# Kernel optimization log

Measured on AMD Instinct MI355X. Metric: run time of the kernel, lower is better.

## Reference

```python
import jax, jax.numpy as jnp
import numpy as np

N_NODES = 50000
BN_EPS = 1e-5


def gcn_conv(x, W, b, src, dst, ew):
    # x: [N, Fin], W: [Fin, Fout]; PyG GCNConv with self loops and edge weights
    xw = x @ W
    loop = jnp.arange(N_NODES)
    s = jnp.concatenate([src, loop])
    d = jnp.concatenate([dst, loop])
    w = jnp.concatenate([ew, jnp.ones((N_NODES,), ew.dtype)])
    deg = jax.ops.segment_sum(w, d, num_segments=N_NODES)
    dinv = jnp.where(deg > 0, jax.lax.rsqrt(deg), 0.0)
    norm = dinv[s] * w * dinv[d]                      # [E+N]
    msg = norm[:, None] * xw[s]                       # [E+N, Fout]
    out = jax.ops.segment_sum(msg, d, num_segments=N_NODES)
    return out + b


def batch_norm(x, gamma, beta):
    mu = jnp.mean(x, axis=0)
    var = jnp.mean(jnp.square(x - mu), axis=0)
    return gamma * (x - mu) * jax.lax.rsqrt(var + BN_EPS) + beta


def setup_inputs() -> dict:
    key = jax.random.key(0)
    ks = jax.random.split(key, 6)
    F_IN, H, C, E = 128, 128, 40, 800000
    x = jax.random.normal(ks[0], (N_NODES, F_IN), jnp.float32)
    edge_index = jax.random.randint(ks[1], (2, E), 0, N_NODES, jnp.int64)
    edge_weight = jax.random.uniform(ks[2], (E,), jnp.float32)
    W1 = jax.random.normal(ks[3], (F_IN, H), jnp.float32) / np.sqrt(F_IN)
    W2 = jax.random.normal(ks[4], (H, H), jnp.float32) / np.sqrt(H)
    W3 = jax.random.normal(ks[5], (H, C), jnp.float32) / np.sqrt(H)
    return {
        "x": x, "edge_index": edge_index, "edge_weight": edge_weight,
        "W1": W1, "b1": jnp.zeros((H,), jnp.float32),
        "gamma1": jnp.ones((H,), jnp.float32), "beta1": jnp.zeros((H,), jnp.float32),
        "W2": W2, "b2": jnp.zeros((H,), jnp.float32),
        "gamma2": jnp.ones((H,), jnp.float32), "beta2": jnp.zeros((H,), jnp.float32),
        "W3": W3, "b3": jnp.zeros((C,), jnp.float32),
    }


def reference(x, edge_index, edge_weight, W1, b1, gamma1, beta1,
              W2, b2, gamma2, beta2, W3, b3):
    src, dst = edge_index[0], edge_index[1]
    h = gcn_conv(x, W1, b1, src, dst, edge_weight)
    h = jax.nn.relu(batch_norm(h, gamma1, beta1))   # dropout = identity (eval)
    h = gcn_conv(h, W2, b2, src, dst, edge_weight)
    h = jax.nn.relu(batch_norm(h, gamma2, beta2))
    h = gcn_conv(h, W3, b3, src, dst, edge_weight)
    return jax.nn.log_softmax(h, axis=-1)
```

## Files before the change

kernel.cpp:

```cpp
#include <hip/hip_runtime.h>
#include <cstdint>
#include <cstddef>

#define N_NODES 50000
#define BN_EPS 1e-5f
#define NPB 256
#define NB ((N_NODES + NPB - 1) / NPB)
#define EPB 2048
#define BN_BLOCKS 128

typedef unsigned int uint32;
typedef unsigned short ushort;

typedef short bf16x8 __attribute__((ext_vector_type(8)));
typedef float f32x4 __attribute__((ext_vector_type(4)));


__device__ inline ushort bf16rn(float f) {
  unsigned int u = __float_as_uint(f);
  u += 0x7fffu + ((u >> 16) & 1u);
  return (ushort)(u >> 16);
}
__device__ inline float unbf(uint32 u) { return __uint_as_float(u << 16); }
__device__ inline float lo16(uint32 u) { return __uint_as_float(u << 16); }
__device__ inline float hi16(uint32 u) { return __uint_as_float(u & 0xffff0000u); }
__device__ inline uint32 pack2(float a, float b) {
  return (uint32)bf16rn(a) | ((uint32)bf16rn(b) << 16);
}


__global__ __launch_bounds__(256) void k_cvtW_all(const float* __restrict__ W1,
    const float* __restrict__ W2, const float* __restrict__ W3,
    ushort* __restrict__ Wt1, ushort* __restrict__ Wt2, ushort* __restrict__ Wt3) {
  int gid = blockIdx.x * 256 + threadIdx.x;
  if (gid < 16384) {
    int c = gid >> 7, k = gid & 127;
    Wt1[c * 128 + k] = bf16rn(W1[(size_t)k * 128 + c]);
  } else if (gid < 32768) {
    int g = gid - 16384, c = g >> 7, k = g & 127;
    Wt2[c * 128 + k] = bf16rn(W2[(size_t)k * 128 + c]);
  } else if (gid < 37888) {
    int g = gid - 32768, c = g >> 7, k = g & 127;
    Wt3[c * 128 + k] = bf16rn(W3[(size_t)k * 40 + c]);
  }
}


__global__ __launch_bounds__(256) void k_ehist(const int* __restrict__ dst, int E,
    int* __restrict__ histB, int* __restrict__ hists, int* __restrict__ done,
    int* __restrict__ rbase, int* __restrict__ cbase, int* __restrict__ start) {
  __shared__ int h[NB];
  for (int i = threadIdx.x; i < NB; i += 256) h[i] = 0;
  __syncthreads();
  int base = blockIdx.x * EPB;
  for (int i = threadIdx.x; i < EPB; i += 256) {
    int e = base + i;
    if (e < E) atomicAdd(&h[dst[e] >> 8], 1);
  }
  __syncthreads();
  for (int i = threadIdx.x; i < NB; i += 256) {
    int v = h[i];
    hists[blockIdx.x * NB + i] = v;
    if (v) atomicAdd(&histB[i], v);
  }
  if (threadIdx.x == 0) {
    __threadfence();
    int old = atomicAdd(done, 1);
    if (old == gridDim.x - 1) {
      __threadfence();
      int r = 0, c = 0;
      for (int b = 0; b < NB; ++b) {
        int npb = (b == NB - 1) ? (N_NODES - b * NPB) : NPB;
        rbase[b] = r; cbase[b] = c;
        r += histB[b]; c += histB[b] + npb;
      }
      rbase[NB] = r;
      start[N_NODES] = c;
    }
  }
}

__global__ __launch_bounds__(256) void k_binA(const int* __restrict__ src,
    const int* __restrict__ dst, const float* __restrict__ ew, int E,
    const int* __restrict__ rbase, const int* __restrict__ hists,
    int* __restrict__ gcur, uint2* __restrict__ bins) {
  __shared__ int gb[NB], cur[NB];
  for (int i = threadIdx.x; i < NB; i += 256) {
    int hv = hists[blockIdx.x * NB + i];
    cur[i] = 0;
    gb[i] = hv ? (rbase[i] + atomicAdd(&gcur[i], hv)) : 0;
  }
  __syncthreads();
  int base = blockIdx.x * EPB;
  for (int i = threadIdx.x; i < EPB; i += 256) {
    int e = base + i;
    if (e < E) {
      int d = dst[e];
      int g = d >> 8;
      int p = gb[g] + atomicAdd(&cur[g], 1);
      bins[p] = make_uint2((uint32)src[e] | ((uint32)(d & 255) << 16),
                           __float_as_uint(ew[e]));
    }
  }
}

__global__ __launch_bounds__(256) void k_binB(const uint2* __restrict__ bins,
    const int* __restrict__ rbase, const int* __restrict__ cbase,
    int* __restrict__ start, float* __restrict__ dinv, uint32* __restrict__ csr) {
  __shared__ int h[256], cur[256], ofs[256], sc[256];
  __shared__ float deg[256];
  int tid = threadIdx.x;
  int b = blockIdx.x;
  int node0 = b << 8;
  int npb = min(NPB, N_NODES - node0);
  h[tid] = 0; deg[tid] = 1.0f;
  __syncthreads();
  int r0 = rbase[b], r1 = rbase[b + 1];
  for (int i = r0 + tid; i < r1; i += 256) {
    uint2 rec = bins[i];
    int dl = (rec.x >> 16) & 255;
    atomicAdd(&h[dl], 1);
    atomicAdd(&deg[dl], __uint_as_float(rec.y));
  }
  __syncthreads();
  int v = (tid < npb) ? 1 + h[tid] : 0;
  sc[tid] = v;
  __syncthreads();
  for (int off = 1; off < 256; off <<= 1) {
    int a = (tid >= off) ? sc[tid - off] : 0;
    __syncthreads();
    sc[tid] += a;
    __syncthreads();
  }
  int cb = cbase[b];
  if (tid < npb) {
    int segBase = cb + sc[tid] - v;
    int node = node0 + tid;
    start[node] = segBase;
    csr[segBase] = (0x3F80u << 16) | (uint32)node;
    dinv[node] = rsqrtf(deg[tid]);
    ofs[tid] = segBase + 1;
    cur[tid] = 0;
  }
  __syncthreads();
  for (int i = r0 + tid; i < r1; i += 256) {
    uint2 rec = bins[i];
    int dl = (rec.x >> 16) & 255;
    int p = ofs[dl] + atomicAdd(&cur[dl], 1);
    csr[p] = ((uint32)bf16rn(__uint_as_float(rec.y)) << 16) | (rec.x & 0xffff);
  }
}

__global__ __launch_bounds__(256) void k_wnorm(uint32* __restrict__ csr,
    const int* __restrict__ start, const float* __restrict__ dinv) {
  int lane = threadIdx.x & 15;
  int node = blockIdx.x * 16 + (threadIdx.x >> 4);
  if (node >= N_NODES) return;
  float di = dinv[node];
  int e0 = start[node], e1 = start[node + 1];
  for (int e = e0 + lane; e < e1; e += 16) {
    uint32 c = csr[e];
    int s = c & 0xffff;
    float w = unbf(c >> 16) * dinv[s] * di;
    csr[e] = ((uint32)bf16rn(w) << 16) | (uint32)s;
  }
}


template <int BNT, typename XT>
__global__ __launch_bounds__(256) void k_mfma(const XT* __restrict__ X,
    const ushort* __restrict__ Wt, const float* __restrict__ ssb,
    ushort* __restrict__ out16, int Fout) {
  __shared__ ushort Xs[64][136];
  __shared__ ushort Bs[BNT * 16][136];
  int tid = threadIdx.x;
  int r0 = blockIdx.x * 64;

  for (int idx = tid; idx < BNT * 16 * 16; idx += 256) {
    int col = idx >> 4;
    int kk = (idx & 15) * 8;
    uint4 v = make_uint4(0, 0, 0, 0);
    if (col < Fout)
      v = *reinterpret_cast<const uint4*>(&Wt[(size_t)col * 128 + kk]);
    *reinterpret_cast<uint4*>(&Bs[col][kk]) = v;
  }

  if (sizeof(XT) == 4) {
    const float* Xf = reinterpret_cast<const float*>(X);
    for (int idx = tid; idx < 2048; idx += 256) {
      int row = idx >> 5;
      int kk = (idx & 31) * 4;
      int gr = r0 + row;
      float4 v = make_float4(0.f, 0.f, 0.f, 0.f);
      if (gr < N_NODES)
        v = *reinterpret_cast<const float4*>(&Xf[(size_t)gr * 128 + kk]);
      ushort4 o;
      o.x = bf16rn(v.x); o.y = bf16rn(v.y); o.z = bf16rn(v.z); o.w = bf16rn(v.w);
      *reinterpret_cast<ushort4*>(&Xs[row][kk]) = o;
    }
  } else {
    const ushort* X16 = reinterpret_cast<const ushort*>(X);
    for (int idx = tid; idx < 1024; idx += 256) {
      int row = idx >> 4;
      int kk = (idx & 15) * 8;
      int gr = r0 + row;
      uint4 v = make_uint4(0, 0, 0, 0);
      if (gr < N_NODES)
        v = *reinterpret_cast<const uint4*>(&X16[(size_t)gr * 128 + kk]);
      if (ssb) {
        float f[8] = { lo16(v.x), hi16(v.x), lo16(v.y), hi16(v.y),
                       lo16(v.z), hi16(v.z), lo16(v.w), hi16(v.w) };
        float4 sc0 = *reinterpret_cast<const float4*>(&ssb[kk]);
        float4 sc1 = *reinterpret_cast<const float4*>(&ssb[kk + 4]);
        float4 sh0 = *reinterpret_cast<const float4*>(&ssb[128 + kk]);
        float4 sh1 = *reinterpret_cast<const float4*>(&ssb[128 + kk + 4]);
        f[0] = fmaxf(0.f, f[0] * sc0.x + sh0.x);
        f[1] = fmaxf(0.f, f[1] * sc0.y + sh0.y);
        f[2] = fmaxf(0.f, f[2] * sc0.z + sh0.z);
        f[3] = fmaxf(0.f, f[3] * sc0.w + sh0.w);
        f[4] = fmaxf(0.f, f[4] * sc1.x + sh1.x);
        f[5] = fmaxf(0.f, f[5] * sc1.y + sh1.y);
        f[6] = fmaxf(0.f, f[6] * sc1.z + sh1.z);
        f[7] = fmaxf(0.f, f[7] * sc1.w + sh1.w);
        v.x = pack2(f[0], f[1]); v.y = pack2(f[2], f[3]);
        v.z = pack2(f[4], f[5]); v.w = pack2(f[6], f[7]);
      }
      *reinterpret_cast<uint4*>(&Xs[row][kk]) = v;
    }
  }
  __syncthreads();

  int lane = tid & 63, wav = tid >> 6;
  int lrow = lane & 15, lk = (lane >> 4) * 8;
  f32x4 acc[BNT];
  #pragma unroll
  for (int ct = 0; ct < BNT; ++ct) acc[ct] = (f32x4){0.f, 0.f, 0.f, 0.f};

  #pragma unroll
  for (int kc = 0; kc < 4; ++kc) {
    int k0 = kc * 32 + lk;
    bf16x8 a = *reinterpret_cast<const bf16x8*>(&Xs[wav * 16 + lrow][k0]);
    #pragma unroll
    for (int ct = 0; ct < BNT; ++ct) {
      bf16x8 b = *reinterpret_cast<const bf16x8*>(&Bs[ct * 16 + lrow][k0]);
      acc[ct] = __builtin_amdgcn_mfma_f32_16x16x32_bf16(a, b, acc[ct], 0, 0, 0);
    }
  }

  int orow = wav * 16 + (lane >> 4) * 4;
  #pragma unroll
  for (int ct = 0; ct < BNT; ++ct) {
    int gc = ct * 16 + lrow;
    if (gc >= Fout) continue;
    #pragma unroll
    for (int i = 0; i < 4; ++i) {
      int gr = r0 + orow + i;
      if (gr < N_NODES) out16[(size_t)gr * Fout + gc] = bf16rn(acc[ct][i]);
    }
  }
}


__global__ __launch_bounds__(256) void k_agg128c(const ushort* __restrict__ xw,
    const float* __restrict__ bias, const int* __restrict__ start,
    const uint32* __restrict__ csr, ushort* __restrict__ out16) {
  int lane = threadIdx.x & 63;
  int node = blockIdx.x * 4 + (threadIdx.x >> 6);
  if (node >= N_NODES) return;
  int sub = lane >> 4;
  int fl  = lane & 15;
  const uint4* rows = (const uint4*)xw;
  float acc[8] = {};
  int e0 = start[node], e1 = start[node + 1];
  int e = e0 + sub;
  for (; e + 12 < e1; e += 16) {
    uint32 c0 = csr[e], c1 = csr[e + 4], c2 = csr[e + 8], c3 = csr[e + 12];
    uint4 v0 = rows[(size_t)(c0 & 0xffff) * 16 + fl];
    uint4 v1 = rows[(size_t)(c1 & 0xffff) * 16 + fl];
    uint4 v2 = rows[(size_t)(c2 & 0xffff) * 16 + fl];
    uint4 v3 = rows[(size_t)(c3 & 0xffff) * 16 + fl];
    float w0 = unbf(c0 >> 16), w1 = unbf(c1 >> 16);
    float w2 = unbf(c2 >> 16), w3 = unbf(c3 >> 16);
    acc[0] += w0 * lo16(v0.x) + w1 * lo16(v1.x) + w2 * lo16(v2.x) + w3 * lo16(v3.x);
    acc[1] += w0 * hi16(v0.x) + w1 * hi16(v1.x) + w2 * hi16(v2.x) + w3 * hi16(v3.x);
    acc[2] += w0 * lo16(v0.y) + w1 * lo16(v1.y) + w2 * lo16(v2.y) + w3 * lo16(v3.y);
    acc[3] += w0 * hi16(v0.y) + w1 * hi16(v1.y) + w2 * hi16(v2.y) + w3 * hi16(v3.y);
    acc[4] += w0 * lo16(v0.z) + w1 * lo16(v1.z) + w2 * lo16(v2.z) + w3 * lo16(v3.z);
    acc[5] += w0 * hi16(v0.z) + w1 * hi16(v1.z) + w2 * hi16(v2.z) + w3 * hi16(v3.z);
    acc[6] += w0 * lo16(v0.w) + w1 * lo16(v1.w) + w2 * lo16(v2.w) + w3 * lo16(v3.w);
    acc[7] += w0 * hi16(v0.w) + w1 * hi16(v1.w) + w2 * hi16(v2.w) + w3 * hi16(v3.w);
  }
  for (; e < e1; e += 4) {
    uint32 c = csr[e];
    float w = unbf(c >> 16);
    uint4 v = rows[(size_t)(c & 0xffff) * 16 + fl];
    acc[0] += w * lo16(v.x); acc[1] += w * hi16(v.x);
    acc[2] += w * lo16(v.y); acc[3] += w * hi16(v.y);
    acc[4] += w * lo16(v.z); acc[5] += w * hi16(v.z);
    acc[6] += w * lo16(v.w); acc[7] += w * hi16(v.w);
  }
  #pragma unroll
  for (int k = 0; k < 8; ++k) acc[k] += __shfl_xor(acc[k], 16);
  #pragma unroll
  for (int k = 0; k < 8; ++k) acc[k] += __shfl_xor(acc[k], 32);
  if (sub == 0) {
    float4 b0 = ((const float4*)bias)[fl * 2];
    float4 b1 = ((const float4*)bias)[fl * 2 + 1];
    acc[0] += b0.x; acc[1] += b0.y; acc[2] += b0.z; acc[3] += b0.w;
    acc[4] += b1.x; acc[5] += b1.y; acc[6] += b1.z; acc[7] += b1.w;
    uint4 o;
    o.x = pack2(acc[0], acc[1]);
    o.y = pack2(acc[2], acc[3]);
    o.z = pack2(acc[4], acc[5]);
    o.w = pack2(acc[6], acc[7]);
    ((uint4*)out16)[(size_t)node * 16 + fl] = o;
  }
}


__global__ __launch_bounds__(256) void k_agg40lsm(const ushort* __restrict__ xw,
    const float* __restrict__ bias, const int* __restrict__ start,
    const uint32* __restrict__ csr, float* __restrict__ out) {
  int lane = threadIdx.x & 63;
  int node = blockIdx.x * 4 + (threadIdx.x >> 6);
  if (node >= N_NODES) return;
  int sub = lane >> 4;
  int fl  = lane & 15;
  bool active = fl < 10;
  int flc = active ? fl : 0;
  const uint2* rows = (const uint2*)xw;
  float acc[4] = {};
  int e0 = start[node], e1 = start[node + 1];
  int e = e0 + sub;
  for (; e + 4 < e1; e += 8) {
    uint32 c0 = csr[e], c1 = csr[e + 4];
    uint2 v0 = rows[(size_t)(c0 & 0xffff) * 10 + flc];
    uint2 v1 = rows[(size_t)(c1 & 0xffff) * 10 + flc];
    float w0 = unbf(c0 >> 16), w1 = unbf(c1 >> 16);
    if (active) {
      acc[0] += w0 * lo16(v0.x) + w1 * lo16(v1.x);
      acc[1] += w0 * hi16(v0.x) + w1 * hi16(v1.x);
      acc[2] += w0 * lo16(v0.y) + w1 * lo16(v1.y);
      acc[3] += w0 * hi16(v0.y) + w1 * hi16(v1.y);
    }
  }
  if (e < e1) {
    uint32 c = csr[e];
    float w = unbf(c >> 16);
    uint2 v = rows[(size_t)(c & 0xffff) * 10 + flc];
    if (active) {
      acc[0] += w * lo16(v.x); acc[1] += w * hi16(v.x);
      acc[2] += w * lo16(v.y); acc[3] += w * hi16(v.y);
    }
  }
  #pragma unroll
  for (int k = 0; k < 4; ++k) acc[k] += __shfl_xor(acc[k], 16);
  #pragma unroll
  for (int k = 0; k < 4; ++k) acc[k] += __shfl_xor(acc[k], 32);
  if (sub == 0) {
    float m = -1e30f, es = 0.f;
    if (active) {
      float4 b = ((const float4*)bias)[fl];
      acc[0] += b.x; acc[1] += b.y; acc[2] += b.z; acc[3] += b.w;
      m = fmaxf(fmaxf(acc[0], acc[1]), fmaxf(acc[2], acc[3]));
    }
    #pragma unroll
    for (int off = 8; off >= 1; off >>= 1) m = fmaxf(m, __shfl_xor(m, off, 16));
    if (active)
      es = expf(acc[0] - m) + expf(acc[1] - m) + expf(acc[2] - m) + expf(acc[3] - m);
    #pragma unroll
    for (int off = 8; off >= 1; off >>= 1) es += __shfl_xor(es, off, 16);
    if (active) {
      float lse = m + logf(es);
      float4 o = make_float4(acc[0] - lse, acc[1] - lse, acc[2] - lse, acc[3] - lse);
      *reinterpret_cast<float4*>(&out[(size_t)node * 40 + fl * 4]) = o;
    }
  }
}


__global__ __launch_bounds__(256) void k_bnstats1(const ushort* __restrict__ x,
    float* __restrict__ partials, int* __restrict__ done,
    const float* __restrict__ gamma, const float* __restrict__ beta,
    float* __restrict__ ssb) {
  int tid = threadIdx.x;
  int fl = tid & 15;
  int rg = tid >> 4;
  float s[8] = {}, q[8] = {};
  const uint4* xv = (const uint4*)x;
  for (int row = blockIdx.x * 16 + rg; row < N_NODES; row += BN_BLOCKS * 16) {
    uint4 v = xv[(size_t)row * 16 + fl];
    float f0 = lo16(v.x), f1 = hi16(v.x), f2 = lo16(v.y), f3 = hi16(v.y);
    float f4 = lo16(v.z), f5 = hi16(v.z), f6 = lo16(v.w), f7 = hi16(v.w);
    s[0] += f0; q[0] += f0 * f0; s[1] += f1; q[1] += f1 * f1;
    s[2] += f2; q[2] += f2 * f2; s[3] += f3; q[3] += f3 * f3;
    s[4] += f4; q[4] += f4 * f4; s[5] += f5; q[5] += f5 * f5;
    s[6] += f6; q[6] += f6 * f6; s[7] += f7; q[7] += f7 * f7;
  }
  __shared__ float ls[256][8];
  __shared__ float lq[256][8];
  #pragma unroll
  for (int j = 0; j < 8; ++j) { ls[tid][j] = s[j]; lq[tid][j] = q[j]; }
  __syncthreads();
  for (int step = 8; step >= 1; step >>= 1) {
    if (rg < step) {
      #pragma unroll
      for (int j = 0; j < 8; ++j) {
        ls[rg * 16 + fl][j] += ls[(rg + step) * 16 + fl][j];
        lq[rg * 16 + fl][j] += lq[(rg + step) * 16 + fl][j];
      }
    }
    __syncthreads();
  }
  if (rg == 0) {
    #pragma unroll
    for (int j = 0; j < 8; ++j) {
      partials[(size_t)blockIdx.x * 256 + fl * 8 + j] = ls[fl][j];
      partials[(size_t)blockIdx.x * 256 + 128 + fl * 8 + j] = lq[fl][j];
    }
  }
  __shared__ int isLast;
  __syncthreads();
  if (tid == 0) {
    __threadfence();
    isLast = (atomicAdd(done, 1) == BN_BLOCKS - 1) ? 1 : 0;
  }
  __syncthreads();
  if (isLast) {
    __threadfence();
    float acc = 0.f;
    for (int b = 0; b < BN_BLOCKS; ++b) acc += partials[(size_t)b * 256 + tid];
    __shared__ float st[256];
    st[tid] = acc;
    __syncthreads();
    if (tid < 128) {
      float inv_n = 1.0f / (float)N_NODES;
      float mu = st[tid] * inv_n;
      float var = st[128 + tid] * inv_n - mu * mu;
      if (var < 0.f) var = 0.f;
      float sc = gamma[tid] * rsqrtf(var + BN_EPS);
      ssb[tid] = sc;
      ssb[128 + tid] = beta[tid] - mu * sc;
    }
  }
}


extern "C" void kernel_launch(void* const* d_in, const int* in_sizes, int n_in,
                              void* d_out, int out_size, void* d_ws, size_t ws_size,
                              hipStream_t stream) {
  const float* x   = (const float*)d_in[0];
  const int*   ei  = (const int*)d_in[1];
  const float* ew  = (const float*)d_in[2];
  const float* W1  = (const float*)d_in[3];
  const float* b1  = (const float*)d_in[4];
  const float* g1  = (const float*)d_in[5];
  const float* be1 = (const float*)d_in[6];
  const float* W2  = (const float*)d_in[7];
  const float* b2  = (const float*)d_in[8];
  const float* g2  = (const float*)d_in[9];
  const float* be2 = (const float*)d_in[10];
  const float* W3  = (const float*)d_in[11];
  const float* b3  = (const float*)d_in[12];
  float* out = (float*)d_out;
  int E = in_sizes[2];
  const int* src = ei;
  const int* dst = ei + E;
  int nblkA = (E + EPB - 1) / EPB;

  char* p = (char*)d_ws;
  auto alloc = [&](size_t bytes) {
    char* r = p; p += (bytes + 255) & ~(size_t)255; return r;
  };
  int*    histB  = (int*)   alloc((size_t)(NB + 1) * 4);
  int*    gcur   = (int*)   alloc((size_t)NB * 4);
  int*    doneE  = (int*)   alloc(4);
  int*    doneB1 = (int*)   alloc(4);
  int*    doneB2 = (int*)   alloc(4);
  size_t zspan = (size_t)((char*)doneB2 + 4 - (char*)histB);
  int*    rbase  = (int*)   alloc((size_t)(NB + 1) * 4);
  int*    cbase  = (int*)   alloc((size_t)NB * 4);
  int*    hists  = (int*)   alloc((size_t)nblkA * NB * 4);
  int*    startA = (int*)   alloc((size_t)(N_NODES + 1) * 4);
  float*  dinv   = (float*) alloc((size_t)N_NODES * 4);
  uint2*  bins   = (uint2*) alloc((size_t)E * 8);
  uint32* csr    = (uint32*)alloc((size_t)(E + N_NODES) * 4);
  float*  parts  = (float*) alloc((size_t)BN_BLOCKS * 256 * 4);
  float*  ssb1   = (float*) alloc(256 * 4);
  float*  ssb2   = (float*) alloc(256 * 4);
  ushort* Wt1    = (ushort*)alloc((size_t)128 * 128 * 2);
  ushort* Wt2    = (ushort*)alloc((size_t)128 * 128 * 2);
  ushort* Wt3    = (ushort*)alloc((size_t)40 * 128 * 2);
  ushort* xw16   = (ushort*)alloc((size_t)N_NODES * 128 * 2);
  ushort* buf16  = (ushort*)alloc((size_t)N_NODES * 128 * 2);

  hipMemsetAsync(histB, 0, zspan, stream);
  k_cvtW_all<<<149, 256, 0, stream>>>(W1, W2, W3, Wt1, Wt2, Wt3);
  k_ehist<<<nblkA, 256, 0, stream>>>(dst, E, histB, hists, doneE, rbase, cbase, startA);
  k_binA<<<nblkA, 256, 0, stream>>>(src, dst, ew, E, rbase, hists, gcur, bins);
  k_binB<<<NB, 256, 0, stream>>>(bins, rbase, cbase, startA, dinv, csr);
  k_wnorm<<<(N_NODES + 15) / 16, 256, 0, stream>>>(csr, startA, dinv);

  int gemmGrid = (N_NODES + 63) / 64;
  int aggGrid = (N_NODES + 3) / 4;

  k_mfma<8, float><<<gemmGrid, 256, 0, stream>>>(x, Wt1, nullptr, xw16, 128);
  k_agg128c<<<aggGrid, 256, 0, stream>>>(xw16, b1, startA, csr, buf16);
  k_bnstats1<<<BN_BLOCKS, 256, 0, stream>>>(buf16, parts, doneB1, g1, be1, ssb1);

  k_mfma<8, ushort><<<gemmGrid, 256, 0, stream>>>(buf16, Wt2, ssb1, xw16, 128);
  k_agg128c<<<aggGrid, 256, 0, stream>>>(xw16, b2, startA, csr, buf16);
  k_bnstats1<<<BN_BLOCKS, 256, 0, stream>>>(buf16, parts, doneB2, g2, be2, ssb2);

  k_mfma<3, ushort><<<gemmGrid, 256, 0, stream>>>(buf16, Wt3, ssb2, xw16, 40);
  k_agg40lsm<<<aggGrid, 256, 0, stream>>>(xw16, b3, startA, csr, out);
}
```

Baseline: 237.8 us.

## Co-launch weight conversion with histogram and layer-1 GEMM with edge binning

Merges independent preprocessing stages into shared launches. Weight conversion now runs in extra blocks of the edge-histogram kernel, and the first-layer GEMM runs in the same grid as the edge-binning pass, selected by block index. This removes two kernel launches and lets unrelated work overlap on the GPU. It also halves the node bucket size to 128, giving more and smaller binB blocks, and doubles the number of BN stats blocks. The catch is that binB still allocates 256-entry shared arrays with only half used, and the fused GEMM block now reserves shared memory for the binning branch as well.

```diff
diff --git a/kernel.cpp b/kernel.cpp
--- a/kernel.cpp
+++ b/kernel.cpp
@@ -4,10 +4,10 @@
 
 #define N_NODES 50000
 #define BN_EPS 1e-5f
-#define NPB 256
+#define NPB 128
 #define NB ((N_NODES + NPB - 1) / NPB)
 #define EPB 2048
-#define BN_BLOCKS 128
+#define BN_BLOCKS 256
 
 typedef unsigned int uint32;
 typedef unsigned short ushort;
@@ -29,33 +29,33 @@
 }
 
 
-__global__ __launch_bounds__(256) void k_cvtW_all(const float* __restrict__ W1,
-    const float* __restrict__ W2, const float* __restrict__ W3,
+__global__ __launch_bounds__(256) void k_cvt_ehist(const int* __restrict__ dst, int E,
+    int nblkA, int* __restrict__ histB, int* __restrict__ hists, int* __restrict__ done,
+    int* __restrict__ rbase, int* __restrict__ cbase, int* __restrict__ start,
+    const float* __restrict__ W1, const float* __restrict__ W2,
+    const float* __restrict__ W3,
     ushort* __restrict__ Wt1, ushort* __restrict__ Wt2, ushort* __restrict__ Wt3) {
-  int gid = blockIdx.x * 256 + threadIdx.x;
-  if (gid < 16384) {
-    int c = gid >> 7, k = gid & 127;
-    Wt1[c * 128 + k] = bf16rn(W1[(size_t)k * 128 + c]);
-  } else if (gid < 32768) {
-    int g = gid - 16384, c = g >> 7, k = g & 127;
-    Wt2[c * 128 + k] = bf16rn(W2[(size_t)k * 128 + c]);
-  } else if (gid < 37888) {
-    int g = gid - 32768, c = g >> 7, k = g & 127;
-    Wt3[c * 128 + k] = bf16rn(W3[(size_t)k * 40 + c]);
-  }
-}
-
-
-__global__ __launch_bounds__(256) void k_ehist(const int* __restrict__ dst, int E,
-    int* __restrict__ histB, int* __restrict__ hists, int* __restrict__ done,
-    int* __restrict__ rbase, int* __restrict__ cbase, int* __restrict__ start) {
+  if ((int)blockIdx.x >= nblkA) {
+    int gid = (blockIdx.x - nblkA) * 256 + threadIdx.x;
+    if (gid < 16384) {
+      int c = gid >> 7, k = gid & 127;
+      Wt1[c * 128 + k] = bf16rn(W1[(size_t)k * 128 + c]);
+    } else if (gid < 32768) {
+      int g = gid - 16384, c = g >> 7, k = g & 127;
+      Wt2[c * 128 + k] = bf16rn(W2[(size_t)k * 128 + c]);
+    } else if (gid < 37888) {
+      int g = gid - 32768, c = g >> 7, k = g & 127;
+      Wt3[c * 128 + k] = bf16rn(W3[(size_t)k * 40 + c]);
+    }
+    return;
+  }
   __shared__ int h[NB];
   for (int i = threadIdx.x; i < NB; i += 256) h[i] = 0;
   __syncthreads();
   int base = blockIdx.x * EPB;
   for (int i = threadIdx.x; i < EPB; i += 256) {
     int e = base + i;
-    if (e < E) atomicAdd(&h[dst[e] >> 8], 1);
+    if (e < E) atomicAdd(&h[dst[e] / NPB], 1);
   }
   __syncthreads();
   for (int i = threadIdx.x; i < NB; i += 256) {
@@ -66,7 +66,7 @@
   if (threadIdx.x == 0) {
     __threadfence();
     int old = atomicAdd(done, 1);
-    if (old == gridDim.x - 1) {
+    if (old == nblkA - 1) {
       __threadfence();
       int r = 0, c = 0;
       for (int b = 0; b < NB; ++b) {
@@ -80,29 +80,91 @@
   }
 }
 
-__global__ __launch_bounds__(256) void k_binA(const int* __restrict__ src,
-    const int* __restrict__ dst, const float* __restrict__ ew, int E,
+
+__global__ __launch_bounds__(256) void k_mfma_binA(
+    const float* __restrict__ X, const ushort* __restrict__ Wt,
+    ushort* __restrict__ out16, int gemmGrid,
+    const int* __restrict__ src, const int* __restrict__ dst,
+    const float* __restrict__ ew, int E,
     const int* __restrict__ rbase, const int* __restrict__ hists,
     int* __restrict__ gcur, uint2* __restrict__ bins) {
-  __shared__ int gb[NB], cur[NB];
-  for (int i = threadIdx.x; i < NB; i += 256) {
-    int hv = hists[blockIdx.x * NB + i];
-    cur[i] = 0;
-    gb[i] = hv ? (rbase[i] + atomicAdd(&gcur[i], hv)) : 0;
-  }
-  __syncthreads();
-  int base = blockIdx.x * EPB;
-  for (int i = threadIdx.x; i < EPB; i += 256) {
-    int e = base + i;
-    if (e < E) {
-      int d = dst[e];
-      int g = d >> 8;
-      int p = gb[g] + atomicAdd(&cur[g], 1);
-      bins[p] = make_uint2((uint32)src[e] | ((uint32)(d & 255) << 16),
-                           __float_as_uint(ew[e]));
-    }
-  }
-}
+  __shared__ __align__(16) char smem[64 * 136 * 2 + 128 * 136 * 2];
+  int tid = threadIdx.x;
+
+  if ((int)blockIdx.x >= gemmGrid) {
+    int blk = blockIdx.x - gemmGrid;
+    int* gb = (int*)smem;
+    int* cur = gb + NB;
+    for (int i = tid; i < NB; i += 256) {
+      int hv = hists[blk * NB + i];
+      cur[i] = 0;
+      gb[i] = hv ? (rbase[i] + atomicAdd(&gcur[i], hv)) : 0;
+    }
+    __syncthreads();
+    int base = blk * EPB;
+    for (int i = tid; i < EPB; i += 256) {
+      int e = base + i;
+      if (e < E) {
+        int d = dst[e];
+        int g = d / NPB;
+        int p = gb[g] + atomicAdd(&cur[g], 1);
+        bins[p] = make_uint2((uint32)src[e] | ((uint32)(d % NPB) << 16),
+                             __float_as_uint(ew[e]));
+      }
+    }
+    return;
+  }
+
+  ushort (*Xs)[136] = (ushort(*)[136])smem;
+  ushort (*Bs)[136] = (ushort(*)[136])(smem + 64 * 136 * 2);
+  int r0 = blockIdx.x * 64;
+
+  for (int idx = tid; idx < 128 * 16; idx += 256) {
+    int col = idx >> 4;
+    int kk = (idx & 15) * 8;
+    uint4 v = *reinterpret_cast<const uint4*>(&Wt[(size_t)col * 128 + kk]);
+    *reinterpret_cast<uint4*>(&Bs[col][kk]) = v;
+  }
+  for (int idx = tid; idx < 2048; idx += 256) {
+    int row = idx >> 5;
+    int kk = (idx & 31) * 4;
+    int gr = r0 + row;
+    float4 v = make_float4(0.f, 0.f, 0.f, 0.f);
+    if (gr < N_NODES)
+      v = *reinterpret_cast<const float4*>(&X[(size_t)gr * 128 + kk]);
+    ushort4 o;
+    o.x = bf16rn(v.x); o.y = bf16rn(v.y); o.z = bf16rn(v.z); o.w = bf16rn(v.w);
+    *reinterpret_cast<ushort4*>(&Xs[row][kk]) = o;
+  }
+  __syncthreads();
+
+  int lane = tid & 63, wav = tid >> 6;
+  int lrow = lane & 15, lk = (lane >> 4) * 8;
+  f32x4 acc[8];
+  #pragma unroll
+  for (int ct = 0; ct < 8; ++ct) acc[ct] = (f32x4){0.f, 0.f, 0.f, 0.f};
+  #pragma unroll
+  for (int kc = 0; kc < 4; ++kc) {
+    int k0 = kc * 32 + lk;
+    bf16x8 a = *reinterpret_cast<const bf16x8*>(&Xs[wav * 16 + lrow][k0]);
+    #pragma unroll
+    for (int ct = 0; ct < 8; ++ct) {
+      bf16x8 b = *reinterpret_cast<const bf16x8*>(&Bs[ct * 16 + lrow][k0]);
+      acc[ct] = __builtin_amdgcn_mfma_f32_16x16x32_bf16(a, b, acc[ct], 0, 0, 0);
+    }
+  }
+  int orow = wav * 16 + (lane >> 4) * 4;
+  #pragma unroll
+  for (int ct = 0; ct < 8; ++ct) {
+    int gc = ct * 16 + lrow;
+    #pragma unroll
+    for (int i = 0; i < 4; ++i) {
+      int gr = r0 + orow + i;
+      if (gr < N_NODES) out16[(size_t)gr * 128 + gc] = bf16rn(acc[ct][i]);
+    }
+  }
+}
+
 
 __global__ __launch_bounds__(256) void k_binB(const uint2* __restrict__ bins,
     const int* __restrict__ rbase, const int* __restrict__ cbase,
@@ -111,7 +173,7 @@
   __shared__ float deg[256];
   int tid = threadIdx.x;
   int b = blockIdx.x;
-  int node0 = b << 8;
+  int node0 = b * NPB;
   int npb = min(NPB, N_NODES - node0);
   h[tid] = 0; deg[tid] = 1.0f;
   __syncthreads();
@@ -167,8 +229,8 @@
 }
 
 
-template <int BNT, typename XT>
-__global__ __launch_bounds__(256) void k_mfma(const XT* __restrict__ X,
+template <int BNT>
+__global__ __launch_bounds__(256) void k_mfma(const ushort* __restrict__ X,
     const ushort* __restrict__ Wt, const float* __restrict__ ssb,
     ushort* __restrict__ out16, int Fout) {
   __shared__ ushort Xs[64][136];
@@ -184,49 +246,30 @@
       v = *reinterpret_cast<const uint4*>(&Wt[(size_t)col * 128 + kk]);
     *reinterpret_cast<uint4*>(&Bs[col][kk]) = v;
   }
-
-  if (sizeof(XT) == 4) {
-    const float* Xf = reinterpret_cast<const float*>(X);
-    for (int idx = tid; idx < 2048; idx += 256) {
-      int row = idx >> 5;
-      int kk = (idx & 31) * 4;
-      int gr = r0 + row;
-      float4 v = make_float4(0.f, 0.f, 0.f, 0.f);
-      if (gr < N_NODES)
-        v = *reinterpret_cast<const float4*>(&Xf[(size_t)gr * 128 + kk]);
-      ushort4 o;
-      o.x = bf16rn(v.x); o.y = bf16rn(v.y); o.z = bf16rn(v.z); o.w = bf16rn(v.w);
-      *reinterpret_cast<ushort4*>(&Xs[row][kk]) = o;
-    }
-  } else {
-    const ushort* X16 = reinterpret_cast<const ushort*>(X);
-    for (int idx = tid; idx < 1024; idx += 256) {
-      int row = idx >> 4;
-      int kk = (idx & 15) * 8;
-      int gr = r0 + row;
-      uint4 v = make_uint4(0, 0, 0, 0);
-      if (gr < N_NODES)
-        v = *reinterpret_cast<const uint4*>(&X16[(size_t)gr * 128 + kk]);
-      if (ssb) {
-        float f[8] = { lo16(v.x), hi16(v.x), lo16(v.y), hi16(v.y),
-                       lo16(v.z), hi16(v.z), lo16(v.w), hi16(v.w) };
-        float4 sc0 = *reinterpret_cast<const float4*>(&ssb[kk]);
-        float4 sc1 = *reinterpret_cast<const float4*>(&ssb[kk + 4]);
-        float4 sh0 = *reinterpret_cast<const float4*>(&ssb[128 + kk]);
-        float4 sh1 = *reinterpret_cast<const float4*>(&ssb[128 + kk + 4]);
-        f[0] = fmaxf(0.f, f[0] * sc0.x + sh0.x);
-        f[1] = fmaxf(0.f, f[1] * sc0.y + sh0.y);
-        f[2] = fmaxf(0.f, f[2] * sc0.z + sh0.z);
-        f[3] = fmaxf(0.f, f[3] * sc0.w + sh0.w);
-        f[4] = fmaxf(0.f, f[4] * sc1.x + sh1.x);
-        f[5] = fmaxf(0.f, f[5] * sc1.y + sh1.y);
-        f[6] = fmaxf(0.f, f[6] * sc1.z + sh1.z);
-        f[7] = fmaxf(0.f, f[7] * sc1.w + sh1.w);
-        v.x = pack2(f[0], f[1]); v.y = pack2(f[2], f[3]);
-        v.z = pack2(f[4], f[5]); v.w = pack2(f[6], f[7]);
-      }
-      *reinterpret_cast<uint4*>(&Xs[row][kk]) = v;
-    }
+  for (int idx = tid; idx < 1024; idx += 256) {
+    int row = idx >> 4;
+    int kk = (idx & 15) * 8;
+    int gr = r0 + row;
+    uint4 v = make_uint4(0, 0, 0, 0);
+    if (gr < N_NODES)
+      v = *reinterpret_cast<const uint4*>(&X[(size_t)gr * 128 + kk]);
+    float f[8] = { lo16(v.x), hi16(v.x), lo16(v.y), hi16(v.y),
+                   lo16(v.z), hi16(v.z), lo16(v.w), hi16(v.w) };
+    float4 sc0 = *reinterpret_cast<const float4*>(&ssb[kk]);
+    float4 sc1 = *reinterpret_cast<const float4*>(&ssb[kk + 4]);
+    float4 sh0 = *reinterpret_cast<const float4*>(&ssb[128 + kk]);
+    float4 sh1 = *reinterpret_cast<const float4*>(&ssb[128 + kk + 4]);
+    f[0] = fmaxf(0.f, f[0] * sc0.x + sh0.x);
+    f[1] = fmaxf(0.f, f[1] * sc0.y + sh0.y);
+    f[2] = fmaxf(0.f, f[2] * sc0.z + sh0.z);
+    f[3] = fmaxf(0.f, f[3] * sc0.w + sh0.w);
+    f[4] = fmaxf(0.f, f[4] * sc1.x + sh1.x);
+    f[5] = fmaxf(0.f, f[5] * sc1.y + sh1.y);
+    f[6] = fmaxf(0.f, f[6] * sc1.z + sh1.z);
+    f[7] = fmaxf(0.f, f[7] * sc1.w + sh1.w);
+    v.x = pack2(f[0], f[1]); v.y = pack2(f[2], f[3]);
+    v.z = pack2(f[4], f[5]); v.w = pack2(f[6], f[7]);
+    *reinterpret_cast<uint4*>(&Xs[row][kk]) = v;
   }
   __syncthreads();
 
@@ -235,7 +278,6 @@
   f32x4 acc[BNT];
   #pragma unroll
   for (int ct = 0; ct < BNT; ++ct) acc[ct] = (f32x4){0.f, 0.f, 0.f, 0.f};
-
   #pragma unroll
   for (int kc = 0; kc < 4; ++kc) {
     int k0 = kc * 32 + lk;
@@ -246,7 +288,6 @@
       acc[ct] = __builtin_amdgcn_mfma_f32_16x16x32_bf16(a, b, acc[ct], 0, 0, 0);
     }
   }
-
   int orow = wav * 16 + (lane >> 4) * 4;
   #pragma unroll
   for (int ct = 0; ct < BNT; ++ct) {
@@ -494,24 +535,24 @@
   ushort* xw16   = (ushort*)alloc((size_t)N_NODES * 128 * 2);
   ushort* buf16  = (ushort*)alloc((size_t)N_NODES * 128 * 2);
 
+  int gemmGrid = (N_NODES + 63) / 64;
+  int aggGrid = (N_NODES + 3) / 4;
+
   hipMemsetAsync(histB, 0, zspan, stream);
-  k_cvtW_all<<<149, 256, 0, stream>>>(W1, W2, W3, Wt1, Wt2, Wt3);
-  k_ehist<<<nblkA, 256, 0, stream>>>(dst, E, histB, hists, doneE, rbase, cbase, startA);
-  k_binA<<<nblkA, 256, 0, stream>>>(src, dst, ew, E, rbase, hists, gcur, bins);
+  k_cvt_ehist<<<nblkA + 148, 256, 0, stream>>>(dst, E, nblkA, histB, hists, doneE,
+      rbase, cbase, startA, W1, W2, W3, Wt1, Wt2, Wt3);
+  k_mfma_binA<<<gemmGrid + nblkA, 256, 0, stream>>>(x, Wt1, xw16, gemmGrid,
+      src, dst, ew, E, rbase, hists, gcur, bins);
   k_binB<<<NB, 256, 0, stream>>>(bins, rbase, cbase, startA, dinv, csr);
   k_wnorm<<<(N_NODES + 15) / 16, 256, 0, stream>>>(csr, startA, dinv);
 
-  int gemmGrid = (N_NODES + 63) / 64;
-  int aggGrid = (N_NODES + 3) / 4;
-
-  k_mfma<8, float><<<gemmGrid, 256, 0, stream>>>(x, Wt1, nullptr, xw16, 128);
   k_agg128c<<<aggGrid, 256, 0, stream>>>(xw16, b1, startA, csr, buf16);
   k_bnstats1<<<BN_BLOCKS, 256, 0, stream>>>(buf16, parts, doneB1, g1, be1, ssb1);
 
-  k_mfma<8, ushort><<<gemmGrid, 256, 0, stream>>>(buf16, Wt2, ssb1, xw16, 128);
+  k_mfma<8><<<gemmGrid, 256, 0, stream>>>(buf16, Wt2, ssb1, xw16, 128);
   k_agg128c<<<aggGrid, 256, 0, stream>>>(xw16, b2, startA, csr, buf16);
   k_bnstats1<<<BN_BLOCKS, 256, 0, stream>>>(buf16, parts, doneB2, g2, be2, ssb2);
 
-  k_mfma<3, ushort><<<gemmGrid, 256, 0, stream>>>(buf16, Wt3, ssb2, xw16, 40);
+  k_mfma<3><<<gemmGrid, 256, 0, stream>>>(buf16, Wt3, ssb2, xw16, 40);
   k_agg40lsm<<<aggGrid, 256, 0, stream>>>(xw16, b3, startA, csr, out);
 }
```

Measured after the change: 241.7 us. No clear change (+1.6%).
